# Performance work log

Measured on AMD Instinct MI355X. Metric: run time of the kernel, lower is better.

## Reference

```python
import jax, jax.numpy as jnp
import numpy as np

N = 100000      # nodes
E = 1600000     # edges
DIN, DH, DOUT = 128, 256, 40


def setup_inputs() -> dict:
    key = jax.random.key(0)
    ks = jax.random.split(key, 24)

    def w(i, fan_in, fan_out):
        s = 1.0 / np.sqrt(fan_in)
        return jax.random.uniform(ks[i], (fan_in, fan_out), jnp.float32, -s, s)

    def b(i, fan_in, fan_out):
        s = 1.0 / np.sqrt(fan_in)
        return jax.random.uniform(ks[i], (fan_out,), jnp.float32, -s, s)

    return {
        "x": jax.random.normal(ks[0], (N, DIN), jnp.float32),
        "edge_index": jax.random.randint(ks[1], (2, E), 0, N, dtype=jnp.int64),
        # updates_continues: Linear(DIN,DH), Linear(DH,DH), Linear(DH,DOUT)
        "Wc0": w(2, DIN, DH),  "bc0": b(3, DIN, DH),
        "Wc1": w(4, DH, DH),   "bc1": b(5, DH, DH),
        "Wc2": w(6, DH, DOUT), "bc2": b(7, DH, DOUT),
        # updates_exit: Linear(DIN,DOUT) x2, Linear(DH,DOUT) x2
        "We0": w(8, DIN, DOUT),  "be0": b(9, DIN, DOUT),
        "We1": w(10, DIN, DOUT), "be1": b(11, DIN, DOUT),
        "We2": w(12, DH, DOUT),  "be2": b(13, DH, DOUT),
        "We3": w(14, DH, DOUT),  "be3": b(15, DH, DOUT),
    }


def _gcn_agg(h, src, dst):
    """Symmetric-normalized GCN aggregation with self-loops: D^-1/2 (A+I) D^-1/2 h."""
    ones = jnp.ones(src.shape[0], h.dtype)
    deg = jax.ops.segment_sum(ones, dst, num_segments=N) + 1.0  # self-loop
    dinv = jax.lax.rsqrt(deg)
    coef = dinv[src] * dinv[dst]                    # [E]
    msgs = h[src] * coef[:, None]                   # [E, d] gather
    out = jax.ops.segment_sum(msgs, dst, num_segments=N)  # scatter-add
    return out + h * (dinv * dinv)[:, None]         # self-loop term


def reference(x, edge_index, Wc0, bc0, Wc1, bc1, Wc2, bc2,
              We0, be0, We1, be1, We2, be2, We3, be3):
    src, dst = edge_index[0], edge_index[1]
    Wc = [(Wc0, bc0), (Wc1, bc1), (Wc2, bc2)]
    We = [(We0, be0), (We1, be1), (We2, be2), (We3, be3)]

    h = x
    outs = [jax.nn.log_softmax(h @ We[0][0] + We[0][1], axis=1)]
    for i in range(3):
        h = _gcn_agg(h, src, dst)
        outs.append(jax.nn.log_softmax(h @ We[i + 1][0] + We[i + 1][1], axis=1))
        h = h @ Wc[i][0] + Wc[i][1]
        if i < 2:
            h = jax.nn.relu(h)  # dropout is identity in eval mode
    return jnp.stack(outs, axis=1)  # [N, num_layers+1, DOUT]
```

## Files before the change

kernel.cpp:

```cpp
#include <hip/hip_runtime.h>

#define NNODES 100000
#define NEDGES 1600000

typedef __attribute__((ext_vector_type(8))) short bf16x8;
typedef __attribute__((ext_vector_type(4))) float f32x4;

__device__ __forceinline__ float bf2f(unsigned v) {
  union { unsigned u; float f; } x; x.u = v << 16; return x.f;
}
__device__ __forceinline__ unsigned short f2bf(float f) {
  union { float f; unsigned u; } x; x.f = f;
  unsigned r = x.u + 0x7fffu + ((x.u >> 16) & 1u);
  return (unsigned short)(r >> 16);
}

__global__ void k_probe(const unsigned* __restrict__ xw, const int* __restrict__ ei,
                        int* __restrict__ flags) {
  __shared__ int cF, cI;
  if (threadIdx.x == 0) { cF = 0; cI = 0; }
  __syncthreads();
  int t = threadIdx.x;
  int hf = 0;
  for (int i = t; i < 2048; i += 256) {
    unsigned lo = xw[i] & 0xffffu;
    unsigned e = (lo >> 7) & 0xffu;
    if (e >= 0xC0u) hf++;
  }
  atomicAdd(&cF, hf);
  int hi = 0;
  if (ei[2 * t + 1] != 0) hi++;
  atomicAdd(&cI, hi);
  __syncthreads();
  if (threadIdx.x == 0) {
    flags[0] = (cF > 32) ? 1 : 0;
    flags[1] = (cI < 16) ? 1 : 0;
  }
}

__device__ __forceinline__ int edge_at(const int* __restrict__ ei, int j, int i64) {
  return i64 ? ei[2 * j] : ei[j];
}

struct CvtParams {
  const void* src[13];
  unsigned short* dst[13];
  int n[13];
};

__global__ void k_cvt(CvtParams p, const int* __restrict__ flags) {
  int a = blockIdx.y;
  int n = p.n[a];
  int f32 = flags[0];
  const float* sf = (const float*)p.src[a];
  const unsigned short* sb = (const unsigned short*)p.src[a];
  unsigned short* d = p.dst[a];
  for (int i = blockIdx.x * blockDim.x + threadIdx.x; i < n; i += gridDim.x * blockDim.x) {
    d[i] = f32 ? f2bf(sf[i]) : sb[i];
  }
}

__global__ void k_transpose(const unsigned short* __restrict__ W,
                            unsigned short* __restrict__ WT, int K) {
  int idx = blockIdx.x * 256 + threadIdx.x;
  if (idx < K * 256) {
    int k = idx >> 8, c = idx & 255;
    WT[c * K + k] = W[idx];
  }
}

template <int K>
__global__ void k_transpose40(const unsigned short* __restrict__ W,
                              unsigned short* __restrict__ WT) {
  int idx = blockIdx.x * 256 + threadIdx.x;
  if (idx < 48 * K) {
    int c = idx / K, k = idx % K;
    WT[idx] = (c < 40) ? W[k * 40 + c] : (unsigned short)0;
  }
}

__global__ void k_zero(int* __restrict__ p, int n) {
  int v = blockIdx.x * blockDim.x + threadIdx.x;
  if (v < n) p[v] = 0;
}

__global__ void k_count(const int* __restrict__ ei, int* __restrict__ cnt,
                        const int* __restrict__ flags) {
  int e = blockIdx.x * blockDim.x + threadIdx.x;
  if (e < NEDGES) {
    int i64 = flags[1];
    int d = edge_at(ei, NEDGES + e, i64);
    if ((unsigned)d < NNODES) atomicAdd(&cnt[d], 1);
  }
}

__global__ void k_dinv(const int* __restrict__ cnt, float* __restrict__ dinv) {
  int v = blockIdx.x * blockDim.x + threadIdx.x;
  if (v < NNODES) dinv[v] = rsqrtf((float)cnt[v] + 1.0f);
}

__global__ void k_psum(const int* __restrict__ cnt, int* __restrict__ bsum) {
  __shared__ int sw[4];
  int t = threadIdx.x;
  int i = blockIdx.x * 256 + t;
  int v = (i < NNODES) ? cnt[i] : 0;
  int x = v;
#pragma unroll
  for (int o = 1; o < 64; o <<= 1) {
    int y = __shfl_up(x, o, 64);
    if ((t & 63) >= o) x += y;
  }
  if ((t & 63) == 63) sw[t >> 6] = x;
  __syncthreads();
  if (t == 0) bsum[blockIdx.x] = sw[0] + sw[1] + sw[2] + sw[3];
}

__global__ void k_bscan(const int* __restrict__ bsum, int* __restrict__ bbase,
                        int* __restrict__ offs) {
  int l = threadIdx.x;
  int base = l * 7;
  int v[7];
  int s = 0;
#pragma unroll
  for (int k = 0; k < 7; ++k) {
    int j = base + k;
    v[k] = (j < 391) ? bsum[j] : 0;
    s += v[k];
  }
  int x = s;
#pragma unroll
  for (int o = 1; o < 64; o <<= 1) {
    int y = __shfl_up(x, o, 64);
    if (l >= o) x += y;
  }
  int excl = x - s;
#pragma unroll
  for (int k = 0; k < 7; ++k) {
    int j = base + k;
    if (j < 391) bbase[j] = excl;
    excl += v[k];
  }
  if (l == 63) offs[NNODES] = x;
}

__global__ void k_offs(const int* __restrict__ cnt, const int* __restrict__ bbase,
                       int* __restrict__ offs, int* __restrict__ cursor) {
  __shared__ int sw[4], swo[4];
  int t = threadIdx.x;
  int i = blockIdx.x * 256 + t;
  int v = (i < NNODES) ? cnt[i] : 0;
  int x = v;
#pragma unroll
  for (int o = 1; o < 64; o <<= 1) {
    int y = __shfl_up(x, o, 64);
    if ((t & 63) >= o) x += y;
  }
  if ((t & 63) == 63) sw[t >> 6] = x;
  __syncthreads();
  if (t == 0) {
    int a = 0;
#pragma unroll
    for (int w = 0; w < 4; ++w) { swo[w] = a; a += sw[w]; }
  }
  __syncthreads();
  if (i < NNODES) {
    int e = bbase[blockIdx.x] + swo[t >> 6] + x - v;
    offs[i] = e;
    cursor[i] = e;
  }
}

__global__ void k_fill(const int* __restrict__ ei, int* __restrict__ cursor,
                       uint2* __restrict__ csr_sc, const float* __restrict__ dinv,
                       const int* __restrict__ flags) {
  int e = blockIdx.x * blockDim.x + threadIdx.x;
  if (e < NEDGES) {
    int i64 = flags[1];
    int s = edge_at(ei, e, i64), d = edge_at(ei, NEDGES + e, i64);
    if ((unsigned)s < NNODES && (unsigned)d < NNODES) {
      int p = atomicAdd(&cursor[d], 1);
      if ((unsigned)p < NEDGES) {
        float c = dinv[s] * dinv[d];
        uint2 rec;
        rec.x = (unsigned)s;
        union { float f; unsigned u; } cu; cu.f = c;
        rec.y = cu.u;
        csr_sc[p] = rec;
      }
    }
  }
}

__device__ __forceinline__ float u2f(unsigned u) {
  union { unsigned u; float f; } x; x.u = u; return x.f;
}

template <int D>
__global__ __launch_bounds__(256) void k_agg(
    const unsigned short* __restrict__ hin, unsigned short* __restrict__ hout,
    const int* __restrict__ offs, const uint2* __restrict__ csr_sc,
    const float* __restrict__ dinv) {
  constexpr int PER = D / 64;
  int w = (blockIdx.x * 256 + threadIdx.x) >> 6;
  int lane = threadIdx.x & 63;
  if (w >= NNODES) return;
  float dv = dinv[w];
  float acc[PER];
  size_t base = (size_t)w * D + lane * PER;
  if (PER == 4) {
    uint2 u = *(const uint2*)(hin + base);
    acc[0] = bf2f(u.x & 0xffffu) * dv * dv;
    acc[1] = bf2f(u.x >> 16) * dv * dv;
    acc[2] = bf2f(u.y & 0xffffu) * dv * dv;
    acc[3] = bf2f(u.y >> 16) * dv * dv;
  } else {
    unsigned u = *(const unsigned*)(hin + base);
    acc[0] = bf2f(u & 0xffffu) * dv * dv;
    acc[1] = bf2f(u >> 16) * dv * dv;
  }
  int b = offs[w], e = offs[w + 1];
  int i = b;
  const unsigned lim = NNODES - 1;
  for (; i + 4 <= e; i += 4) {
    uint2 m0 = csr_sc[i], m1 = csr_sc[i + 1], m2 = csr_sc[i + 2], m3 = csr_sc[i + 3];
    const unsigned short* p0 = hin + (size_t)(m0.x < lim ? m0.x : lim) * D + lane * PER;
    const unsigned short* p1 = hin + (size_t)(m1.x < lim ? m1.x : lim) * D + lane * PER;
    const unsigned short* p2 = hin + (size_t)(m2.x < lim ? m2.x : lim) * D + lane * PER;
    const unsigned short* p3 = hin + (size_t)(m3.x < lim ? m3.x : lim) * D + lane * PER;
    if (PER == 4) {
      uint2 u0 = *(const uint2*)p0;
      uint2 u1 = *(const uint2*)p1;
      uint2 u2 = *(const uint2*)p2;
      uint2 u3 = *(const uint2*)p3;
      float c0 = u2f(m0.y), c1 = u2f(m1.y), c2 = u2f(m2.y), c3 = u2f(m3.y);
      acc[0] += c0 * bf2f(u0.x & 0xffffu);
      acc[1] += c0 * bf2f(u0.x >> 16);
      acc[2] += c0 * bf2f(u0.y & 0xffffu);
      acc[3] += c0 * bf2f(u0.y >> 16);
      acc[0] += c1 * bf2f(u1.x & 0xffffu);
      acc[1] += c1 * bf2f(u1.x >> 16);
      acc[2] += c1 * bf2f(u1.y & 0xffffu);
      acc[3] += c1 * bf2f(u1.y >> 16);
      acc[0] += c2 * bf2f(u2.x & 0xffffu);
      acc[1] += c2 * bf2f(u2.x >> 16);
      acc[2] += c2 * bf2f(u2.y & 0xffffu);
      acc[3] += c2 * bf2f(u2.y >> 16);
      acc[0] += c3 * bf2f(u3.x & 0xffffu);
      acc[1] += c3 * bf2f(u3.x >> 16);
      acc[2] += c3 * bf2f(u3.y & 0xffffu);
      acc[3] += c3 * bf2f(u3.y >> 16);
    } else {
      unsigned u0 = *(const unsigned*)p0;
      unsigned u1 = *(const unsigned*)p1;
      unsigned u2 = *(const unsigned*)p2;
      unsigned u3 = *(const unsigned*)p3;
      float c0 = u2f(m0.y), c1 = u2f(m1.y), c2 = u2f(m2.y), c3 = u2f(m3.y);
      acc[0] += c0 * bf2f(u0 & 0xffffu);
      acc[1] += c0 * bf2f(u0 >> 16);
      acc[0] += c1 * bf2f(u1 & 0xffffu);
      acc[1] += c1 * bf2f(u1 >> 16);
      acc[0] += c2 * bf2f(u2 & 0xffffu);
      acc[1] += c2 * bf2f(u2 >> 16);
      acc[0] += c3 * bf2f(u3 & 0xffffu);
      acc[1] += c3 * bf2f(u3 >> 16);
    }
  }
  for (; i < e; ++i) {
    uint2 m = csr_sc[i];
    float c = u2f(m.y);
    size_t sb = (size_t)(m.x < lim ? m.x : lim) * D + lane * PER;
    if (PER == 4) {
      uint2 u = *(const uint2*)(hin + sb);
      acc[0] += c * bf2f(u.x & 0xffffu);
      acc[1] += c * bf2f(u.x >> 16);
      acc[2] += c * bf2f(u.y & 0xffffu);
      acc[3] += c * bf2f(u.y >> 16);
    } else {
      unsigned u = *(const unsigned*)(hin + sb);
      acc[0] += c * bf2f(u & 0xffffu);
      acc[1] += c * bf2f(u >> 16);
    }
  }
  if (PER == 4) {
    uint2 o;
    o.x = (unsigned)f2bf(acc[0]) | ((unsigned)f2bf(acc[1]) << 16);
    o.y = (unsigned)f2bf(acc[2]) | ((unsigned)f2bf(acc[3]) << 16);
    *(uint2*)(hout + base) = o;
  } else {
    *(unsigned*)(hout + base) =
        (unsigned)f2bf(acc[0]) | ((unsigned)f2bf(acc[1]) << 16);
  }
}

__global__ __launch_bounds__(256) void k_agg40(
    const unsigned short* __restrict__ P, const int* __restrict__ offs,
    const uint2* __restrict__ csr_sc, const float* __restrict__ dinv,
    const unsigned short* __restrict__ bias, float* __restrict__ outp) {
  int w = (blockIdx.x * 256 + threadIdx.x) >> 6;
  int lane = threadIdx.x & 63;
  if (w >= NNODES) return;
  float dv = dinv[w];
  float a0 = 0.f, a1 = 0.f;
  const unsigned lim = NNODES - 1;
  if (lane < 20) {
    unsigned u = *(const unsigned*)(P + (size_t)w * 40 + lane * 2);
    a0 = bf2f(u & 0xffffu) * dv * dv;
    a1 = bf2f(u >> 16) * dv * dv;
  }
  int b = offs[w], e = offs[w + 1];
  int i = b;
  for (; i + 4 <= e; i += 4) {
    uint2 m0 = csr_sc[i], m1 = csr_sc[i + 1], m2 = csr_sc[i + 2], m3 = csr_sc[i + 3];
    if (lane < 20) {
      unsigned u0 = *(const unsigned*)(P + (size_t)(m0.x < lim ? m0.x : lim) * 40 + lane * 2);
      unsigned u1 = *(const unsigned*)(P + (size_t)(m1.x < lim ? m1.x : lim) * 40 + lane * 2);
      unsigned u2 = *(const unsigned*)(P + (size_t)(m2.x < lim ? m2.x : lim) * 40 + lane * 2);
      unsigned u3 = *(const unsigned*)(P + (size_t)(m3.x < lim ? m3.x : lim) * 40 + lane * 2);
      float c0 = u2f(m0.y), c1 = u2f(m1.y), c2 = u2f(m2.y), c3 = u2f(m3.y);
      a0 += c0 * bf2f(u0 & 0xffffu);
      a1 += c0 * bf2f(u0 >> 16);
      a0 += c1 * bf2f(u1 & 0xffffu);
      a1 += c1 * bf2f(u1 >> 16);
      a0 += c2 * bf2f(u2 & 0xffffu);
      a1 += c2 * bf2f(u2 >> 16);
      a0 += c3 * bf2f(u3 & 0xffffu);
      a1 += c3 * bf2f(u3 >> 16);
    }
  }
  for (; i < e; ++i) {
    uint2 m = csr_sc[i];
    if (lane < 20) {
      unsigned u = *(const unsigned*)(P + (size_t)(m.x < lim ? m.x : lim) * 40 + lane * 2);
      float c = u2f(m.y);
      a0 += c * bf2f(u & 0xffffu);
      a1 += c * bf2f(u >> 16);
    }
  }
  if (lane < 20) {
    a0 += bf2f((unsigned)bias[lane * 2]);
    a1 += bf2f((unsigned)bias[lane * 2 + 1]);
  }
  float m = (lane < 20) ? fmaxf(a0, a1) : -1e30f;
#pragma unroll
  for (int o = 16; o > 0; o >>= 1) m = fmaxf(m, __shfl_xor(m, o, 32));
  float ss = (lane < 20) ? (expf(a0 - m) + expf(a1 - m)) : 0.f;
#pragma unroll
  for (int o = 16; o > 0; o >>= 1) ss += __shfl_xor(ss, o, 32);
  float ls = logf(ss) + m;
  if (lane < 20) {
    float2 o2;
    o2.x = a0 - ls;
    o2.y = a1 - ls;
    *(float2*)(outp + (size_t)w * 160 + lane * 2) = o2;
  }
}

template <int K>
__global__ __launch_bounds__(256) void k_mlp_mfma(
    const unsigned short* __restrict__ A, const unsigned short* __restrict__ WT,
    const unsigned short* __restrict__ bias, unsigned short* __restrict__ out) {
  __shared__ short As[128 * 40];
  __shared__ short Bs[128 * 40];
  const int t = threadIdx.x;
  const int lane = t & 63, wv = t >> 6;
  const int m0 = blockIdx.x * 128;
  const int c0 = blockIdx.y * 128;
  const int mw = (wv >> 1) * 64, nw = (wv & 1) * 64;
  const int lr = lane & 15, lq = lane >> 4;

  f32x4 acc[4][4];
#pragma unroll
  for (int i = 0; i < 4; ++i)
#pragma unroll
    for (int j = 0; j < 4; ++j) acc[i][j] = (f32x4)0.f;

  for (int kc = 0; kc < K; kc += 32) {
    __syncthreads();
#pragma unroll
    for (int it = 0; it < 2; ++it) {
      int idx = t + it * 256;
      int row = idx >> 2, seg = idx & 3;
      uint4 u = make_uint4(0, 0, 0, 0);
      int gr = m0 + row;
      if (gr < NNODES) u = *(const uint4*)(A + (size_t)gr * K + kc + seg * 8);
      *(uint4*)&As[row * 40 + seg * 8] = u;
      uint4 v = *(const uint4*)(WT + (size_t)(c0 + row) * K + kc + seg * 8);
      *(uint4*)&Bs[row * 40 + seg * 8] = v;
    }
    __syncthreads();
    bf16x8 af[4], bfr[4];
#pragma unroll
    for (int i = 0; i < 4; ++i)
      af[i] = *(const bf16x8*)&As[(mw + 16 * i + lr) * 40 + lq * 8];
#pragma unroll
    for (int j = 0; j < 4; ++j)
      bfr[j] = *(const bf16x8*)&Bs[(nw + 16 * j + lr) * 40 + lq * 8];
#pragma unroll
    for (int i = 0; i < 4; ++i)
#pragma unroll
      for (int j = 0; j < 4; ++j)
        acc[i][j] = __builtin_amdgcn_mfma_f32_16x16x32_bf16(af[i], bfr[j], acc[i][j], 0, 0, 0);
  }

  float bv[4];
#pragma unroll
  for (int j = 0; j < 4; ++j) bv[j] = bf2f((unsigned)bias[c0 + nw + 16 * j + lr]);
#pragma unroll
  for (int i = 0; i < 4; ++i) {
    int rbase = m0 + mw + 16 * i + lq * 4;
#pragma unroll
    for (int r = 0; r < 4; ++r) {
      int row = rbase + r;
      if (row < NNODES) {
#pragma unroll
        for (int j = 0; j < 4; ++j) {
          int col = c0 + nw + 16 * j + lr;
          float v = fmaxf(acc[i][j][r] + bv[j], 0.f);
          out[(size_t)row * 256 + col] = f2bf(v);
        }
      }
    }
  }
}

template <int K, bool SOFTMAX>
__global__ __launch_bounds__(256) void k_exit_mfma(
    const unsigned short* __restrict__ A, const unsigned short* __restrict__ WT,
    const unsigned short* __restrict__ bias, float* __restrict__ outp,
    unsigned short* __restrict__ Pout) {
  __shared__ short As[256 * 40];
  __shared__ short Bs[48 * 40];
  const int t = threadIdx.x;
  const int lane = t & 63, wv = t >> 6;
  const int m0 = blockIdx.x * 256;
  const int mw = wv * 64;
  const int lr = lane & 15, lq = lane >> 4;

  f32x4 acc[4][3];
#pragma unroll
  for (int i = 0; i < 4; ++i)
#pragma unroll
    for (int j = 0; j < 3; ++j) acc[i][j] = (f32x4)0.f;

  for (int kc = 0; kc < K; kc += 32) {
    __syncthreads();
#pragma unroll
    for (int it = 0; it < 4; ++it) {
      int idx = t + it * 256;
      int row = idx >> 2, seg = idx & 3;
      uint4 u = make_uint4(0, 0, 0, 0);
      int gr = m0 + row;
      if (gr < NNODES) u = *(const uint4*)(A + (size_t)gr * K + kc + seg * 8);
      *(uint4*)&As[row * 40 + seg * 8] = u;
    }
    if (t < 192) {
      int row = t >> 2, seg = t & 3;
      uint4 v = *(const uint4*)(WT + (size_t)row * K + kc + seg * 8);
      *(uint4*)&Bs[row * 40 + seg * 8] = v;
    }
    __syncthreads();
    bf16x8 af[4], bfr[3];
#pragma unroll
    for (int i = 0; i < 4; ++i)
      af[i] = *(const bf16x8*)&As[(mw + 16 * i + lr) * 40 + lq * 8];
#pragma unroll
    for (int j = 0; j < 3; ++j)
      bfr[j] = *(const bf16x8*)&Bs[(16 * j + lr) * 40 + lq * 8];
#pragma unroll
    for (int i = 0; i < 4; ++i)
#pragma unroll
      for (int j = 0; j < 3; ++j)
        acc[i][j] = __builtin_amdgcn_mfma_f32_16x16x32_bf16(af[i], bfr[j], acc[i][j], 0, 0, 0);
  }

  if (SOFTMAX) {
    float bv0 = bf2f((unsigned)bias[lr]);
    float bv1 = bf2f((unsigned)bias[16 + lr]);
    float bv2 = (lr < 8) ? bf2f((unsigned)bias[32 + lr]) : 0.f;
#pragma unroll
    for (int i = 0; i < 4; ++i) {
#pragma unroll
      for (int r = 0; r < 4; ++r) {
        int row = m0 + mw + 16 * i + lq * 4 + r;
        float v0 = acc[i][0][r] + bv0;
        float v1 = acc[i][1][r] + bv1;
        float v2 = (lr < 8) ? (acc[i][2][r] + bv2) : -1e30f;
        float m = fmaxf(fmaxf(v0, v1), v2);
#pragma unroll
        for (int o = 8; o > 0; o >>= 1) m = fmaxf(m, __shfl_xor(m, o, 16));
        float ss = expf(v0 - m) + expf(v1 - m) + ((lr < 8) ? expf(v2 - m) : 0.f);
#pragma unroll
        for (int o = 8; o > 0; o >>= 1) ss += __shfl_xor(ss, o, 16);
        float ls = logf(ss) + m;
        if (row < NNODES) {
          outp[(size_t)row * 160 + lr] = v0 - ls;
          outp[(size_t)row * 160 + 16 + lr] = v1 - ls;
          if (lr < 8) outp[(size_t)row * 160 + 32 + lr] = v2 - ls;
        }
      }
    }
  } else {
#pragma unroll
    for (int i = 0; i < 4; ++i) {
#pragma unroll
      for (int r = 0; r < 4; ++r) {
        int row = m0 + mw + 16 * i + lq * 4 + r;
        if (row < NNODES) {
          Pout[(size_t)row * 40 + lr] = f2bf(acc[i][0][r]);
          Pout[(size_t)row * 40 + 16 + lr] = f2bf(acc[i][1][r]);
          if (lr < 8) Pout[(size_t)row * 40 + 32 + lr] = f2bf(acc[i][2][r]);
        }
      }
    }
  }
}

extern "C" void kernel_launch(void* const* d_in, const int* in_sizes, int n_in,
                              void* d_out, int out_size, void* d_ws, size_t ws_size,
                              hipStream_t stream) {
  const void* x_raw   = d_in[0];
  const int* ei       = (const int*)d_in[1];
  float* out          = (float*)d_out;

  char* ws = (char*)d_ws;
  int*   flags    = (int*)(ws + 0);
  int*   bsum     = (int*)(ws + 1024);
  int*   bbase    = (int*)(ws + 2816);
  int*   cnt      = (int*)(ws + 8192);
  int*   offs     = (int*)(ws + 524288);
  int*   cursor   = (int*)(ws + 1048576);
  float* dinv     = (float*)(ws + 1572864);
  uint2* csr_sc   = (uint2*)(ws + 2097152);
  unsigned short* xb = (unsigned short*)(ws + 16777216);
  unsigned short* wb = (unsigned short*)(ws + 45088768);
  unsigned short* hA = (unsigned short*)(ws + 48234496);
  unsigned short* hB = (unsigned short*)(ws + 100663296);
  unsigned short* P  = xb;

  unsigned short* Wc0 = wb + 0;
  unsigned short* bc0 = wb + 32768;
  unsigned short* Wc1 = wb + 33024;
  unsigned short* bc1 = wb + 98560;
  unsigned short* We0 = wb + 98816;
  unsigned short* be0 = wb + 103936;
  unsigned short* We1 = wb + 103976;
  unsigned short* be1 = wb + 109096;
  unsigned short* We2 = wb + 109136;
  unsigned short* be2 = wb + 119376;
  unsigned short* We3 = wb + 119416;
  unsigned short* be3 = wb + 129656;
  unsigned short* WTc0  = wb + 131072;
  unsigned short* WTc1  = wb + 163840;
  unsigned short* WT40e0 = wb + 229376;
  unsigned short* WT40e1 = wb + 235520;
  unsigned short* WT40e2 = wb + 241664;
  unsigned short* WT40e3 = wb + 253952;

  dim3 B(256);
  k_probe<<<dim3(1), B, 0, stream>>>((const unsigned*)x_raw, ei, flags);
  k_zero<<<dim3(391), B, 0, stream>>>(cnt, NNODES);

  CvtParams p;
  const int srcIdx[13] = {0, 2, 3, 4, 5, 8, 9, 10, 11, 12, 13, 14, 15};
  unsigned short* dsts[13] = {xb, Wc0, bc0, Wc1, bc1, We0, be0, We1, be1, We2, be2, We3, be3};
  const int ns[13] = {NNODES * 128, 128 * 256, 256, 256 * 256, 256,
                      128 * 40, 40, 128 * 40, 40, 256 * 40, 40, 256 * 40, 40};
  for (int i = 0; i < 13; ++i) { p.src[i] = d_in[srcIdx[i]]; p.dst[i] = dsts[i]; p.n[i] = ns[i]; }
  k_cvt<<<dim3(1024, 13), B, 0, stream>>>(p, flags);
  k_transpose<<<dim3(128), B, 0, stream>>>(Wc0, WTc0, 128);
  k_transpose<<<dim3(256), B, 0, stream>>>(Wc1, WTc1, 256);
  k_transpose40<128><<<dim3(24), B, 0, stream>>>(We0, WT40e0);
  k_transpose40<128><<<dim3(24), B, 0, stream>>>(We1, WT40e1);
  k_transpose40<256><<<dim3(48), B, 0, stream>>>(We2, WT40e2);
  k_transpose40<256><<<dim3(48), B, 0, stream>>>(We3, WT40e3);

  k_count<<<dim3(6250), B, 0, stream>>>(ei, cnt, flags);
  k_dinv<<<dim3(391), B, 0, stream>>>(cnt, dinv);
  k_psum<<<dim3(391), B, 0, stream>>>(cnt, bsum);
  k_bscan<<<dim3(1), dim3(64), 0, stream>>>(bsum, bbase, offs);
  k_offs<<<dim3(391), B, 0, stream>>>(cnt, bbase, offs, cursor);
  k_fill<<<dim3(6250), B, 0, stream>>>(ei, cursor, csr_sc, dinv, flags);

  k_exit_mfma<128, true><<<dim3(391), B, 0, stream>>>(xb, WT40e0, be0, out + 0 * 40, nullptr);
  k_agg<128><<<dim3(25000), B, 0, stream>>>(xb, hA, offs, csr_sc, dinv);
  k_exit_mfma<128, true><<<dim3(391), B, 0, stream>>>(hA, WT40e1, be1, out + 1 * 40, nullptr);
  k_mlp_mfma<128><<<dim3(782, 2), B, 0, stream>>>(hA, WTc0, bc0, hB);
  k_agg<256><<<dim3(25000), B, 0, stream>>>(hB, hA, offs, csr_sc, dinv);
  k_exit_mfma<256, true><<<dim3(391), B, 0, stream>>>(hA, WT40e2, be2, out + 2 * 40, nullptr);
  k_mlp_mfma<256><<<dim3(782, 2), B, 0, stream>>>(hA, WTc1, bc1, hB);
  k_exit_mfma<256, false><<<dim3(391), B, 0, stream>>>(hB, WT40e3, nullptr, nullptr, P);
  k_agg40<<<dim3(25000), B, 0, stream>>>(P, offs, csr_sc, dinv, be3, out + 3 * 40);
}
```

Measured before the change: 747.6 us.

## Split features into 16-wide planes and aggregate per plane with XCD-aware blocks

Stores node features in planar layout: 16-column bf16 slabs, each holding all nodes. Aggregation kernels then walk one plane per block, with blocks mapped so each XCD's L2 sees one plane. The goal is for gathered rows to stay cache-resident. The per-edge coefficient is replaced by pre-scaling features by dinv in the producing GEMMs, so the CSR stores only 4-byte source indices. The final 40-wide aggregation writes fp32 to a scratch buffer, and a separate log-softmax kernel reads it. This adds an extra kernel pass, and the plane layout makes GEMM loads and stores strided.

```diff
diff --git a/kernel.cpp b/kernel.cpp
--- a/kernel.cpp
+++ b/kernel.cpp
@@ -2,9 +2,11 @@
 
 #define NNODES 100000
 #define NEDGES 1600000
+#define PLANE_ELT ((size_t)NNODES * 16)
 
 typedef __attribute__((ext_vector_type(8))) short bf16x8;
 typedef __attribute__((ext_vector_type(4))) float f32x4;
+typedef __attribute__((ext_vector_type(2))) float f32x2;
 
 __device__ __forceinline__ float bf2f(unsigned v) {
   union { unsigned u; float f; } x; x.u = v << 16; return x.f;
@@ -56,7 +58,13 @@
   const unsigned short* sb = (const unsigned short*)p.src[a];
   unsigned short* d = p.dst[a];
   for (int i = blockIdx.x * blockDim.x + threadIdx.x; i < n; i += gridDim.x * blockDim.x) {
-    d[i] = f32 ? f2bf(sf[i]) : sb[i];
+    unsigned short val = f32 ? f2bf(sf[i]) : sb[i];
+    if (a == 0) {
+      int v = i >> 7, c = i & 127;
+      d[(size_t)(c >> 4) * PLANE_ELT + (size_t)v * 16 + (c & 15)] = val;
+    } else {
+      d[i] = val;
+    }
   }
 }
 
@@ -171,201 +179,144 @@
 }
 
 __global__ void k_fill(const int* __restrict__ ei, int* __restrict__ cursor,
-                       uint2* __restrict__ csr_sc, const float* __restrict__ dinv,
-                       const int* __restrict__ flags) {
+                       int* __restrict__ csr_src, const int* __restrict__ flags) {
   int e = blockIdx.x * blockDim.x + threadIdx.x;
   if (e < NEDGES) {
     int i64 = flags[1];
     int s = edge_at(ei, e, i64), d = edge_at(ei, NEDGES + e, i64);
     if ((unsigned)s < NNODES && (unsigned)d < NNODES) {
       int p = atomicAdd(&cursor[d], 1);
-      if ((unsigned)p < NEDGES) {
-        float c = dinv[s] * dinv[d];
-        uint2 rec;
-        rec.x = (unsigned)s;
-        union { float f; unsigned u; } cu; cu.f = c;
-        rec.y = cu.u;
-        csr_sc[p] = rec;
+      if ((unsigned)p < NEDGES) csr_src[p] = s;
+    }
+  }
+}
+
+template <int NP, bool GDINV, bool OUTF32>
+__global__ __launch_bounds__(256) void k_aggp(
+    const unsigned short* __restrict__ IP, unsigned short* __restrict__ OPu,
+    const int* __restrict__ offs, const int* __restrict__ csr_src,
+    const float* __restrict__ dinv) {
+  int b = blockIdx.x;
+  int plane, j0, gsz, gidx;
+  if (NP == 8) {
+    plane = b & 7; j0 = b >> 3; gsz = 1; gidx = 0;
+  } else if (NP == 16) {
+    const int half = 8 * 2500;
+    int ph = (b >= half) ? 1 : 0;
+    int bb = b - ph * half;
+    plane = (bb & 7) + (ph << 3); j0 = bb >> 3; gsz = 1; gidx = 0;
+  } else {
+    int xcd = b & 7;
+    plane = xcd % 3;
+    gidx = xcd / 3;
+    gsz = (plane < 2) ? 3 : 2;
+    j0 = b >> 3;
+  }
+  const int JSTEP = (NP == 3) ? 1250 : 2500;
+  const int wvi = threadIdx.x >> 6;
+  const int lane = threadIdx.x & 63;
+  const int grp = lane >> 3, cl = lane & 7;
+  const unsigned short* ip = IP + (size_t)plane * PLANE_ELT;
+
+  for (int j = j0;; j += JSTEP) {
+    int nblk = j * gsz + gidx;
+    if (nblk >= 25000) break;
+    int v = nblk * 4 + wvi;
+    float dv = dinv[v];
+    unsigned us = *(const unsigned*)(ip + (size_t)v * 16 + (cl << 1));
+    float sc = GDINV ? dv : 1.f;
+    float acc0 = (grp == 0) ? sc * bf2f(us & 0xffffu) : 0.f;
+    float acc1 = (grp == 0) ? sc * bf2f(us >> 16) : 0.f;
+    int b0 = offs[v];
+    int deg = offs[v + 1] - b0;
+    int i = 0;
+    for (; i + 16 <= deg; i += 16) {
+      int s0 = __builtin_nontemporal_load(csr_src + b0 + i + grp);
+      int s1 = __builtin_nontemporal_load(csr_src + b0 + i + 8 + grp);
+      unsigned u0 = *(const unsigned*)(ip + (size_t)s0 * 16 + (cl << 1));
+      unsigned u1 = *(const unsigned*)(ip + (size_t)s1 * 16 + (cl << 1));
+      float w0 = GDINV ? dinv[s0] : 1.f;
+      float w1 = GDINV ? dinv[s1] : 1.f;
+      acc0 += w0 * bf2f(u0 & 0xffffu);
+      acc1 += w0 * bf2f(u0 >> 16);
+      acc0 += w1 * bf2f(u1 & 0xffffu);
+      acc1 += w1 * bf2f(u1 >> 16);
+    }
+    for (; i < deg; i += 8) {
+      int e = i + grp;
+      int ee = (e < deg) ? e : (deg - 1);
+      int src = __builtin_nontemporal_load(csr_src + b0 + ee);
+      float w = (e < deg) ? (GDINV ? dinv[src] : 1.f) : 0.f;
+      unsigned u = *(const unsigned*)(ip + (size_t)src * 16 + (cl << 1));
+      acc0 += w * bf2f(u & 0xffffu);
+      acc1 += w * bf2f(u >> 16);
+    }
+#pragma unroll
+    for (int o = 8; o < 64; o <<= 1) {
+      acc0 += __shfl_xor(acc0, o, 64);
+      acc1 += __shfl_xor(acc1, o, 64);
+    }
+    if (grp == 0) {
+      if (OUTF32) {
+        float* outf = (float*)OPu;
+        f32x2 val;
+        val.x = dv * acc0;
+        val.y = dv * acc1;
+        __builtin_nontemporal_store(
+            val, (f32x2*)(outf + (size_t)plane * PLANE_ELT + (size_t)v * 16 + (cl << 1)));
+      } else {
+        unsigned r = (unsigned)f2bf(dv * acc0) | ((unsigned)f2bf(dv * acc1) << 16);
+        __builtin_nontemporal_store(
+            r, (unsigned*)(OPu + (size_t)plane * PLANE_ELT + (size_t)v * 16 + (cl << 1)));
       }
     }
   }
 }
 
-__device__ __forceinline__ float u2f(unsigned u) {
-  union { unsigned u; float f; } x; x.u = u; return x.f;
-}
-
-template <int D>
-__global__ __launch_bounds__(256) void k_agg(
-    const unsigned short* __restrict__ hin, unsigned short* __restrict__ hout,
-    const int* __restrict__ offs, const uint2* __restrict__ csr_sc,
-    const float* __restrict__ dinv) {
-  constexpr int PER = D / 64;
-  int w = (blockIdx.x * 256 + threadIdx.x) >> 6;
-  int lane = threadIdx.x & 63;
-  if (w >= NNODES) return;
-  float dv = dinv[w];
-  float acc[PER];
-  size_t base = (size_t)w * D + lane * PER;
-  if (PER == 4) {
-    uint2 u = *(const uint2*)(hin + base);
-    acc[0] = bf2f(u.x & 0xffffu) * dv * dv;
-    acc[1] = bf2f(u.x >> 16) * dv * dv;
-    acc[2] = bf2f(u.y & 0xffffu) * dv * dv;
-    acc[3] = bf2f(u.y >> 16) * dv * dv;
-  } else {
-    unsigned u = *(const unsigned*)(hin + base);
-    acc[0] = bf2f(u & 0xffffu) * dv * dv;
-    acc[1] = bf2f(u >> 16) * dv * dv;
-  }
-  int b = offs[w], e = offs[w + 1];
-  int i = b;
-  const unsigned lim = NNODES - 1;
-  for (; i + 4 <= e; i += 4) {
-    uint2 m0 = csr_sc[i], m1 = csr_sc[i + 1], m2 = csr_sc[i + 2], m3 = csr_sc[i + 3];
-    const unsigned short* p0 = hin + (size_t)(m0.x < lim ? m0.x : lim) * D + lane * PER;
-    const unsigned short* p1 = hin + (size_t)(m1.x < lim ? m1.x : lim) * D + lane * PER;
-    const unsigned short* p2 = hin + (size_t)(m2.x < lim ? m2.x : lim) * D + lane * PER;
-    const unsigned short* p3 = hin + (size_t)(m3.x < lim ? m3.x : lim) * D + lane * PER;
-    if (PER == 4) {
-      uint2 u0 = *(const uint2*)p0;
-      uint2 u1 = *(const uint2*)p1;
-      uint2 u2 = *(const uint2*)p2;
-      uint2 u3 = *(const uint2*)p3;
-      float c0 = u2f(m0.y), c1 = u2f(m1.y), c2 = u2f(m2.y), c3 = u2f(m3.y);
-      acc[0] += c0 * bf2f(u0.x & 0xffffu);
-      acc[1] += c0 * bf2f(u0.x >> 16);
-      acc[2] += c0 * bf2f(u0.y & 0xffffu);
-      acc[3] += c0 * bf2f(u0.y >> 16);
-      acc[0] += c1 * bf2f(u1.x & 0xffffu);
-      acc[1] += c1 * bf2f(u1.x >> 16);
-      acc[2] += c1 * bf2f(u1.y & 0xffffu);
-      acc[3] += c1 * bf2f(u1.y >> 16);
-      acc[0] += c2 * bf2f(u2.x & 0xffffu);
-      acc[1] += c2 * bf2f(u2.x >> 16);
-      acc[2] += c2 * bf2f(u2.y & 0xffffu);
-      acc[3] += c2 * bf2f(u2.y >> 16);
-      acc[0] += c3 * bf2f(u3.x & 0xffffu);
-      acc[1] += c3 * bf2f(u3.x >> 16);
-      acc[2] += c3 * bf2f(u3.y & 0xffffu);
-      acc[3] += c3 * bf2f(u3.y >> 16);
-    } else {
-      unsigned u0 = *(const unsigned*)p0;
-      unsigned u1 = *(const unsigned*)p1;
-      unsigned u2 = *(const unsigned*)p2;
-      unsigned u3 = *(const unsigned*)p3;
-      float c0 = u2f(m0.y), c1 = u2f(m1.y), c2 = u2f(m2.y), c3 = u2f(m3.y);
-      acc[0] += c0 * bf2f(u0 & 0xffffu);
-      acc[1] += c0 * bf2f(u0 >> 16);
-      acc[0] += c1 * bf2f(u1 & 0xffffu);
-      acc[1] += c1 * bf2f(u1 >> 16);
-      acc[0] += c2 * bf2f(u2 & 0xffffu);
-      acc[1] += c2 * bf2f(u2 >> 16);
-      acc[0] += c3 * bf2f(u3 & 0xffffu);
-      acc[1] += c3 * bf2f(u3 >> 16);
-    }
-  }
-  for (; i < e; ++i) {
-    uint2 m = csr_sc[i];
-    float c = u2f(m.y);
-    size_t sb = (size_t)(m.x < lim ? m.x : lim) * D + lane * PER;
-    if (PER == 4) {
-      uint2 u = *(const uint2*)(hin + sb);
-      acc[0] += c * bf2f(u.x & 0xffffu);
-      acc[1] += c * bf2f(u.x >> 16);
-      acc[2] += c * bf2f(u.y & 0xffffu);
-      acc[3] += c * bf2f(u.y >> 16);
-    } else {
-      unsigned u = *(const unsigned*)(hin + sb);
-      acc[0] += c * bf2f(u & 0xffffu);
-      acc[1] += c * bf2f(u >> 16);
-    }
-  }
-  if (PER == 4) {
-    uint2 o;
-    o.x = (unsigned)f2bf(acc[0]) | ((unsigned)f2bf(acc[1]) << 16);
-    o.y = (unsigned)f2bf(acc[2]) | ((unsigned)f2bf(acc[3]) << 16);
-    *(uint2*)(hout + base) = o;
-  } else {
-    *(unsigned*)(hout + base) =
-        (unsigned)f2bf(acc[0]) | ((unsigned)f2bf(acc[1]) << 16);
-  }
-}
-
-__global__ __launch_bounds__(256) void k_agg40(
-    const unsigned short* __restrict__ P, const int* __restrict__ offs,
-    const uint2* __restrict__ csr_sc, const float* __restrict__ dinv,
-    const unsigned short* __restrict__ bias, float* __restrict__ outp) {
-  int w = (blockIdx.x * 256 + threadIdx.x) >> 6;
-  int lane = threadIdx.x & 63;
-  if (w >= NNODES) return;
-  float dv = dinv[w];
+__global__ __launch_bounds__(256) void k_ls40(
+    const float* __restrict__ O40f, const unsigned short* __restrict__ bias,
+    float* __restrict__ outp) {
+  int t = threadIdx.x;
+  int wvi = t >> 6, lane = t & 63;
+  int half = lane >> 5, lact = lane & 31;
+  int v = blockIdx.x * 8 + wvi * 2 + half;
+  if (v >= NNODES) return;
+  bool act = lact < 20;
+  int plane = lact >> 3, cl = lact & 7;
+  int col0 = plane * 16 + cl * 2;
   float a0 = 0.f, a1 = 0.f;
-  const unsigned lim = NNODES - 1;
-  if (lane < 20) {
-    unsigned u = *(const unsigned*)(P + (size_t)w * 40 + lane * 2);
-    a0 = bf2f(u & 0xffffu) * dv * dv;
-    a1 = bf2f(u >> 16) * dv * dv;
-  }
-  int b = offs[w], e = offs[w + 1];
-  int i = b;
-  for (; i + 4 <= e; i += 4) {
-    uint2 m0 = csr_sc[i], m1 = csr_sc[i + 1], m2 = csr_sc[i + 2], m3 = csr_sc[i + 3];
-    if (lane < 20) {
-      unsigned u0 = *(const unsigned*)(P + (size_t)(m0.x < lim ? m0.x : lim) * 40 + lane * 2);
-      unsigned u1 = *(const unsigned*)(P + (size_t)(m1.x < lim ? m1.x : lim) * 40 + lane * 2);
-      unsigned u2 = *(const unsigned*)(P + (size_t)(m2.x < lim ? m2.x : lim) * 40 + lane * 2);
-      unsigned u3 = *(const unsigned*)(P + (size_t)(m3.x < lim ? m3.x : lim) * 40 + lane * 2);
-      float c0 = u2f(m0.y), c1 = u2f(m1.y), c2 = u2f(m2.y), c3 = u2f(m3.y);
-      a0 += c0 * bf2f(u0 & 0xffffu);
-      a1 += c0 * bf2f(u0 >> 16);
-      a0 += c1 * bf2f(u1 & 0xffffu);
-      a1 += c1 * bf2f(u1 >> 16);
-      a0 += c2 * bf2f(u2 & 0xffffu);
-      a1 += c2 * bf2f(u2 >> 16);
-      a0 += c3 * bf2f(u3 & 0xffffu);
-      a1 += c3 * bf2f(u3 >> 16);
-    }
-  }
-  for (; i < e; ++i) {
-    uint2 m = csr_sc[i];
-    if (lane < 20) {
-      unsigned u = *(const unsigned*)(P + (size_t)(m.x < lim ? m.x : lim) * 40 + lane * 2);
-      float c = u2f(m.y);
-      a0 += c * bf2f(u & 0xffffu);
-      a1 += c * bf2f(u >> 16);
-    }
-  }
-  if (lane < 20) {
-    a0 += bf2f((unsigned)bias[lane * 2]);
-    a1 += bf2f((unsigned)bias[lane * 2 + 1]);
-  }
-  float m = (lane < 20) ? fmaxf(a0, a1) : -1e30f;
+  if (act) {
+    f32x2 u = *(const f32x2*)(O40f + (size_t)plane * PLANE_ELT + (size_t)v * 16 + (cl << 1));
+    a0 = u.x + bf2f((unsigned)bias[col0]);
+    a1 = u.y + bf2f((unsigned)bias[col0 + 1]);
+  }
+  float m = act ? fmaxf(a0, a1) : -1e30f;
 #pragma unroll
   for (int o = 16; o > 0; o >>= 1) m = fmaxf(m, __shfl_xor(m, o, 32));
-  float ss = (lane < 20) ? (expf(a0 - m) + expf(a1 - m)) : 0.f;
+  float ss = act ? (expf(a0 - m) + expf(a1 - m)) : 0.f;
 #pragma unroll
   for (int o = 16; o > 0; o >>= 1) ss += __shfl_xor(ss, o, 32);
   float ls = logf(ss) + m;
-  if (lane < 20) {
+  if (act) {
     float2 o2;
     o2.x = a0 - ls;
     o2.y = a1 - ls;
-    *(float2*)(outp + (size_t)w * 160 + lane * 2) = o2;
-  }
-}
-
-template <int K>
+    *(float2*)(outp + (size_t)v * 160 + col0) = o2;
+  }
+}
+
+template <int K, bool SCALE>
 __global__ __launch_bounds__(256) void k_mlp_mfma(
     const unsigned short* __restrict__ A, const unsigned short* __restrict__ WT,
-    const unsigned short* __restrict__ bias, unsigned short* __restrict__ out) {
+    const unsigned short* __restrict__ bias, unsigned short* __restrict__ out,
+    const float* __restrict__ dinv) {
   __shared__ short As[128 * 40];
   __shared__ short Bs[128 * 40];
   const int t = threadIdx.x;
-  const int lane = t & 63, wv = t >> 6;
+  const int lane = t & 63, wvq = t >> 6;
   const int m0 = blockIdx.x * 128;
   const int c0 = blockIdx.y * 128;
-  const int mw = (wv >> 1) * 64, nw = (wv & 1) * 64;
+  const int mw = (wvq >> 1) * 64, nw = (wvq & 1) * 64;
   const int lr = lane & 15, lq = lane >> 4;
 
   f32x4 acc[4][4];
@@ -380,12 +331,14 @@
     for (int it = 0; it < 2; ++it) {
       int idx = t + it * 256;
       int row = idx >> 2, seg = idx & 3;
+      int cc = kc + seg * 8;
       uint4 u = make_uint4(0, 0, 0, 0);
       int gr = m0 + row;
-      if (gr < NNODES) u = *(const uint4*)(A + (size_t)gr * K + kc + seg * 8);
+      if (gr < NNODES)
+        u = *(const uint4*)(A + (size_t)(cc >> 4) * PLANE_ELT + (size_t)gr * 16 + (cc & 15));
       *(uint4*)&As[row * 40 + seg * 8] = u;
-      uint4 v = *(const uint4*)(WT + (size_t)(c0 + row) * K + kc + seg * 8);
-      *(uint4*)&Bs[row * 40 + seg * 8] = v;
+      uint4 w = *(const uint4*)(WT + (size_t)(c0 + row) * K + cc);
+      *(uint4*)&Bs[row * 40 + seg * 8] = w;
     }
     __syncthreads();
     bf16x8 af[4], bfr[4];
@@ -412,11 +365,12 @@
     for (int r = 0; r < 4; ++r) {
       int row = rbase + r;
       if (row < NNODES) {
+        float s = SCALE ? dinv[row] : 1.f;
 #pragma unroll
         for (int j = 0; j < 4; ++j) {
           int col = c0 + nw + 16 * j + lr;
-          float v = fmaxf(acc[i][j][r] + bv[j], 0.f);
-          out[(size_t)row * 256 + col] = f2bf(v);
+          float vv = fmaxf(acc[i][j][r] + bv[j], 0.f) * s;
+          out[(size_t)(col >> 4) * PLANE_ELT + (size_t)row * 16 + (col & 15)] = f2bf(vv);
         }
       }
     }
@@ -427,13 +381,13 @@
 __global__ __launch_bounds__(256) void k_exit_mfma(
     const unsigned short* __restrict__ A, const unsigned short* __restrict__ WT,
     const unsigned short* __restrict__ bias, float* __restrict__ outp,
-    unsigned short* __restrict__ Pout) {
+    unsigned short* __restrict__ Pout, const float* __restrict__ dinv) {
   __shared__ short As[256 * 40];
   __shared__ short Bs[48 * 40];
   const int t = threadIdx.x;
-  const int lane = t & 63, wv = t >> 6;
+  const int lane = t & 63, wvq = t >> 6;
   const int m0 = blockIdx.x * 256;
-  const int mw = wv * 64;
+  const int mw = wvq * 64;
   const int lr = lane & 15, lq = lane >> 4;
 
   f32x4 acc[4][3];
@@ -448,15 +402,17 @@
     for (int it = 0; it < 4; ++it) {
       int idx = t + it * 256;
       int row = idx >> 2, seg = idx & 3;
+      int cc = kc + seg * 8;
       uint4 u = make_uint4(0, 0, 0, 0);
       int gr = m0 + row;
-      if (gr < NNODES) u = *(const uint4*)(A + (size_t)gr * K + kc + seg * 8);
+      if (gr < NNODES)
+        u = *(const uint4*)(A + (size_t)(cc >> 4) * PLANE_ELT + (size_t)gr * 16 + (cc & 15));
       *(uint4*)&As[row * 40 + seg * 8] = u;
     }
     if (t < 192) {
       int row = t >> 2, seg = t & 3;
-      uint4 v = *(const uint4*)(WT + (size_t)row * K + kc + seg * 8);
-      *(uint4*)&Bs[row * 40 + seg * 8] = v;
+      uint4 w = *(const uint4*)(WT + (size_t)row * K + kc + seg * 8);
+      *(uint4*)&Bs[row * 40 + seg * 8] = w;
     }
     __syncthreads();
     bf16x8 af[4], bfr[3];
@@ -506,9 +462,11 @@
       for (int r = 0; r < 4; ++r) {
         int row = m0 + mw + 16 * i + lq * 4 + r;
         if (row < NNODES) {
-          Pout[(size_t)row * 40 + lr] = f2bf(acc[i][0][r]);
-          Pout[(size_t)row * 40 + 16 + lr] = f2bf(acc[i][1][r]);
-          if (lr < 8) Pout[(size_t)row * 40 + 32 + lr] = f2bf(acc[i][2][r]);
+          float s = dinv[row];
+          Pout[(size_t)row * 16 + lr] = f2bf(acc[i][0][r] * s);
+          Pout[PLANE_ELT + (size_t)row * 16 + lr] = f2bf(acc[i][1][r] * s);
+          Pout[2 * PLANE_ELT + (size_t)row * 16 + lr] =
+              (lr < 8) ? f2bf(acc[i][2][r] * s) : (unsigned short)0;
         }
       }
     }
@@ -530,12 +488,13 @@
   int*   offs     = (int*)(ws + 524288);
   int*   cursor   = (int*)(ws + 1048576);
   float* dinv     = (float*)(ws + 1572864);
-  uint2* csr_sc   = (uint2*)(ws + 2097152);
-  unsigned short* xb = (unsigned short*)(ws + 16777216);
-  unsigned short* wb = (unsigned short*)(ws + 45088768);
-  unsigned short* hA = (unsigned short*)(ws + 48234496);
-  unsigned short* hB = (unsigned short*)(ws + 100663296);
-  unsigned short* P  = xb;
+  int*   csr_src  = (int*)(ws + 2097152);
+  unsigned short* xpl = (unsigned short*)(ws + 16777216);
+  unsigned short* wb  = (unsigned short*)(ws + 45088768);
+  unsigned short* hAp = (unsigned short*)(ws + 48234496);
+  unsigned short* hBp = (unsigned short*)(ws + 100663296);
+  unsigned short* Pp  = xpl;
+  float* O40f = (float*)(ws + 48234496);
 
   unsigned short* Wc0 = wb + 0;
   unsigned short* bc0 = wb + 32768;
@@ -562,7 +521,7 @@
 
   CvtParams p;
   const int srcIdx[13] = {0, 2, 3, 4, 5, 8, 9, 10, 11, 12, 13, 14, 15};
-  unsigned short* dsts[13] = {xb, Wc0, bc0, Wc1, bc1, We0, be0, We1, be1, We2, be2, We3, be3};
+  unsigned short* dsts[13] = {xpl, Wc0, bc0, Wc1, bc1, We0, be0, We1, be1, We2, be2, We3, be3};
   const int ns[13] = {NNODES * 128, 128 * 256, 256, 256 * 256, 256,
                       128 * 40, 40, 128 * 40, 40, 256 * 40, 40, 256 * 40, 40};
   for (int i = 0; i < 13; ++i) { p.src[i] = d_in[srcIdx[i]]; p.dst[i] = dsts[i]; p.n[i] = ns[i]; }
@@ -579,15 +538,16 @@
   k_psum<<<dim3(391), B, 0, stream>>>(cnt, bsum);
   k_bscan<<<dim3(1), dim3(64), 0, stream>>>(bsum, bbase, offs);
   k_offs<<<dim3(391), B, 0, stream>>>(cnt, bbase, offs, cursor);
-  k_fill<<<dim3(6250), B, 0, stream>>>(ei, cursor, csr_sc, dinv, flags);
-
-  k_exit_mfma<128, true><<<dim3(391), B, 0, stream>>>(xb, WT40e0, be0, out + 0 * 40, nullptr);
-  k_agg<128><<<dim3(25000), B, 0, stream>>>(xb, hA, offs, csr_sc, dinv);
-  k_exit_mfma<128, true><<<dim3(391), B, 0, stream>>>(hA, WT40e1, be1, out + 1 * 40, nullptr);
-  k_mlp_mfma<128><<<dim3(782, 2), B, 0, stream>>>(hA, WTc0, bc0, hB);
-  k_agg<256><<<dim3(25000), B, 0, stream>>>(hB, hA, offs, csr_sc, dinv);
-  k_exit_mfma<256, true><<<dim3(391), B, 0, stream>>>(hA, WT40e2, be2, out + 2 * 40, nullptr);
-  k_mlp_mfma<256><<<dim3(782, 2), B, 0, stream>>>(hA, WTc1, bc1, hB);
-  k_exit_mfma<256, false><<<dim3(391), B, 0, stream>>>(hB, WT40e3, nullptr, nullptr, P);
-  k_agg40<<<dim3(25000), B, 0, stream>>>(P, offs, csr_sc, dinv, be3, out + 3 * 40);
-}
+  k_fill<<<dim3(6250), B, 0, stream>>>(ei, cursor, csr_src, flags);
+
+  k_exit_mfma<128, true><<<dim3(391), B, 0, stream>>>(xpl, WT40e0, be0, out + 0 * 40, nullptr, dinv);
+  k_aggp<8, true, false><<<dim3(20000), B, 0, stream>>>(xpl, hAp, offs, csr_src, dinv);
+  k_exit_mfma<128, true><<<dim3(391), B, 0, stream>>>(hAp, WT40e1, be1, out + 1 * 40, nullptr, dinv);
+  k_mlp_mfma<128, true><<<dim3(782, 2), B, 0, stream>>>(hAp, WTc0, bc0, hBp, dinv);
+  k_aggp<16, false, false><<<dim3(40000), B, 0, stream>>>(hBp, hAp, offs, csr_src, dinv);
+  k_exit_mfma<256, true><<<dim3(391), B, 0, stream>>>(hAp, WT40e2, be2, out + 2 * 40, nullptr, dinv);
+  k_mlp_mfma<256, false><<<dim3(782, 2), B, 0, stream>>>(hAp, WTc1, bc1, hBp, nullptr);
+  k_exit_mfma<256, false><<<dim3(391), B, 0, stream>>>(hBp, WT40e3, nullptr, nullptr, Pp, dinv);
+  k_aggp<3, false, true><<<dim3(10000), B, 0, stream>>>(Pp, (unsigned short*)O40f, offs, csr_src, dinv);
+  k_ls40<<<dim3(12500), B, 0, stream>>>(O40f, be3, out + 3 * 40);
+}
```

Result: slower. 1.354 ms (+81.1%).
